# Performance work log

Measured on AMD Instinct MI355X. Metric: run time of the kernel, lower is better.

## Reference

```python
import jax, jax.numpy as jnp
import numpy as np

B, H, W, C = 32, 56, 56, 192
WS, SHIFT, HEADS = 7, 3, 6
HID = 4 * C
N = WS * WS
NW = (H // WS) * (W // WS)
EPS = 1e-5


def _rel_index():
    ch, cw = np.meshgrid(np.arange(WS), np.arange(WS), indexing='ij')
    coords = np.stack([ch.ravel(), cw.ravel()])  # [2, N]
    rel = coords[:, :, None] - coords[:, None, :]  # [2, N, N]
    rel = rel.transpose(1, 2, 0)
    rel[:, :, 0] += WS - 1
    rel[:, :, 1] += WS - 1
    rel[:, :, 0] *= 2 * WS - 1
    return rel.sum(-1).astype(np.int32)  # [N, N]


def _attn_mask():
    img = np.zeros((H, W), np.float32)
    sl = (slice(0, -WS), slice(-WS, -SHIFT), slice(-SHIFT, None))
    cnt = 0
    for hs in sl:
        for ws_ in sl:
            img[hs, ws_] = cnt
            cnt += 1
    mw = img.reshape(H // WS, WS, W // WS, WS).transpose(0, 2, 1, 3).reshape(-1, N)
    m = mw[:, None, :] - mw[:, :, None]
    return np.where(m != 0, -100.0, 0.0).astype(np.float32)  # [NW, N, N]


def setup_inputs() -> dict:
    key = jax.random.key(0)
    ks = jax.random.split(key, 16)
    r = lambda k, s, sc: (jax.random.normal(k, s, jnp.float32) * sc)
    return {
        'x': r(ks[0], (B, H * W, C), 1.0),
        'norm1_w': jnp.ones((C,), jnp.float32),
        'norm1_b': jnp.zeros((C,), jnp.float32),
        'qkv_w': r(ks[1], (C, 3 * C), 0.02),
        'qkv_b': jnp.zeros((3 * C,), jnp.float32),
        'bias_table': r(ks[2], ((2 * WS - 1) ** 2, HEADS), 0.02),
        'proj_w': r(ks[3], (C, C), 0.02),
        'proj_b': jnp.zeros((C,), jnp.float32),
        'norm2_w': jnp.ones((C,), jnp.float32),
        'norm2_b': jnp.zeros((C,), jnp.float32),
        'fc1_w': r(ks[4], (C, HID), 0.02),
        'fc1_b': jnp.zeros((HID,), jnp.float32),
        'fc2_w': r(ks[5], (HID, C), 0.02),
        'fc2_b': jnp.zeros((C,), jnp.float32),
        'attn_mask': jnp.asarray(_attn_mask()),
        'rel_index': jnp.asarray(_rel_index()),
    }


def _ln(x, w, b):
    mu = jnp.mean(x, -1, keepdims=True)
    var = jnp.mean(jnp.square(x - mu), -1, keepdims=True)
    return (x - mu) * jax.lax.rsqrt(var + EPS) * w + b


def reference(x, norm1_w, norm1_b, qkv_w, qkv_b, bias_table, proj_w, proj_b,
              norm2_w, norm2_b, fc1_w, fc1_b, fc2_w, fc2_b, attn_mask, rel_index):
    shortcut = x
    h = _ln(x, norm1_w, norm1_b).reshape(B, H, W, C)
    # cyclic shift
    h = jnp.roll(h, shift=(-SHIFT, -SHIFT), axis=(1, 2))
    # window partition -> (B*NW, N, C)
    h = h.reshape(B, H // WS, WS, W // WS, WS, C).transpose(0, 1, 3, 2, 4, 5)
    h = h.reshape(B * NW, N, C)
    # attention
    qkv = (h @ qkv_w + qkv_b).reshape(B * NW, N, 3, HEADS, C // HEADS)
    qkv = qkv.transpose(2, 0, 3, 1, 4)  # [3, B_, heads, N, d]
    q, k, v = qkv[0], qkv[1], qkv[2]
    scale = (C // HEADS) ** -0.5
    attn = jnp.einsum('bhnd,bhmd->bhnm', q * scale, k)
    bias = bias_table[rel_index].transpose(2, 0, 1)  # [heads, N, N]
    attn = attn + bias[None]
    attn = attn.reshape(B, NW, HEADS, N, N) + attn_mask[None, :, None]
    attn = jax.nn.softmax(attn.reshape(B * NW, HEADS, N, N), axis=-1)
    o = jnp.einsum('bhnm,bhmd->bhnd', attn, v)
    o = o.transpose(0, 2, 1, 3).reshape(B * NW, N, C)
    o = o @ proj_w + proj_b
    # window reverse
    o = o.reshape(B, H // WS, W // WS, WS, WS, C).transpose(0, 1, 3, 2, 4, 5)
    o = o.reshape(B, H, W, C)
    o = jnp.roll(o, shift=(SHIFT, SHIFT), axis=(1, 2)).reshape(B, H * W, C)
    x = shortcut + o
    # MLP (exact GELU, like torch nn.GELU)
    m = _ln(x, norm2_w, norm2_b)
    m = jax.nn.gelu(m @ fc1_w + fc1_b, approximate=False) @ fc2_w + fc2_b
    return x + m
```

## Files before the change

kernel.cpp:

```cpp
#include <hip/hip_runtime.h>
#include <math.h>

#define B_    32
#define HH    56
#define WW_   56
#define C_    192
#define WS_   7
#define SHIFT_ 3
#define HEADS_ 6
#define DH    32
#define N_    49
#define NWIN  2048
#define ROWS  100352
#define HID_  768
#define QKVN  576

typedef __bf16 bfr;
typedef __bf16 bf8 __attribute__((ext_vector_type(8)));
typedef __bf16 bf4 __attribute__((ext_vector_type(4)));
typedef float  f32x4 __attribute__((ext_vector_type(4)));

#define MFMA16(a,b,c) __builtin_amdgcn_mfma_f32_16x16x32_bf16(a,b,c,0,0,0)

#define OQW   0
#define OPW   110592
#define OW1   147456
#define OW2   294912
#define OBM   442368
#define WTOT  442368
#define BMTOT 1572864

__global__ __launch_bounds__(256) void k_prep(
    const float* __restrict__ qkvw, const float* __restrict__ projw,
    const float* __restrict__ w1,   const float* __restrict__ w2,
    bfr* __restrict__ wsp)
{
  int idx = blockIdx.x*256 + threadIdx.x;
  if (idx >= WTOT) return;
  if (idx < OPW)      { int i=idx;      int n=i/192, k=i%192; wsp[idx] = (bfr)qkvw[k*QKVN + n]; }
  else if (idx < OW1) { int i=idx-OPW;  int n=i/192, k=i%192; wsp[idx] = (bfr)projw[k*C_ + n]; }
  else if (idx < OW2) { int i=idx-OW1;  int n=i/192, k=i%192; wsp[idx] = (bfr)w1[k*HID_ + n]; }
  else                { int i=idx-OW2;  int n=i/768, k=i%768; wsp[idx] = (bfr)w2[k*C_ + n]; }
}

__global__ __launch_bounds__(256) void k_prep2(
    const float* __restrict__ btab, const int* __restrict__ rel,
    const float* __restrict__ mask, bfr* __restrict__ bm)
{
  int idx = blockIdx.x*256 + threadIdx.x;
  if (idx >= BMTOT) return;
  int row = idx & 63, col = (idx>>6) & 63, wi = (idx>>12) & 63, head = idx>>18;
  float v = -1e30f;
  if (row < N_ && col < N_) {
    int e = row*N_ + col;
    v = btab[rel[e]*HEADS_ + head] + mask[(size_t)wi*N_*N_ + e];
  }
  bm[idx] = (bfr)v;
}

#define SM_HS 0
#define SM_QS 25600
#define SM_KS 34816
#define SM_VT 44032
#define SM_P  53248
#define SM_OV 62464
#define SM_SR 71680
#define SM1_TOT 71936
#define HSP 200

__global__ __launch_bounds__(256, 2) void k_attn(
    const float* __restrict__ x,
    const float* __restrict__ n1w, const float* __restrict__ n1b,
    const bfr*   __restrict__ wsp,
    const float* __restrict__ qkvb,
    const float* __restrict__ projb,
    float* __restrict__ out)
{
  __shared__ char smem[SM1_TOT];
  bfr*   hs    = (bfr*)(smem + SM_HS);
  bfr*   qs    = (bfr*)(smem + SM_QS);
  bfr*   ks    = (bfr*)(smem + SM_KS);
  bfr*   vT    = (bfr*)(smem + SM_VT);
  bfr*   P     = (bfr*)(smem + SM_P);
  bfr*   ov2   = (bfr*)(smem + SM_OV);
  int*   srows = (int*)(smem + SM_SR);
  float* pj    = (float*)smem;

  const f32x4 ZERO4 = {0.f, 0.f, 0.f, 0.f};

  int win  = blockIdx.x;
  int tid  = threadIdx.x;
  int lane = tid & 63, wave = tid >> 6;
  int ln15 = lane & 15, quad = lane >> 4;
  int wi   = win & 63;

  if (tid < N_) {
    int bb = win >> 6;
    int wh = wi >> 3, ww = wi & 7;
    int th = tid / WS_, tw = tid % WS_;
    int sh = wh*WS_ + th + SHIFT_; if (sh >= HH) sh -= HH;
    int sw = ww*WS_ + tw + SHIFT_; if (sw >= WW_) sw -= WW_;
    srows[tid] = bb*HH*WW_ + sh*WW_ + sw;
  }
  {
    int* hz = (int*)(hs + 49*HSP);
    for (int i = tid; i < 15*HSP/2; i += 256) hz[i] = 0;
  }
  __syncthreads();
  for (int r = wave; r < N_; r += 4) {
    const float* xr = x + (size_t)srows[r]*C_;
    float v0 = xr[lane], v1 = xr[lane+64], v2 = xr[lane+128];
    float s = v0+v1+v2, q = v0*v0+v1*v1+v2*v2;
    #pragma unroll
    for (int m = 32; m; m >>= 1) { s += __shfl_xor(s, m); q += __shfl_xor(q, m); }
    float mu = s*(1.f/C_), var = q*(1.f/C_) - mu*mu;
    float rs = rsqrtf(var + 1e-5f);
    hs[r*HSP + lane]     = (bfr)((v0-mu)*rs*n1w[lane]     + n1b[lane]);
    hs[r*HSP + lane+64]  = (bfr)((v1-mu)*rs*n1w[lane+64]  + n1b[lane+64]);
    hs[r*HSP + lane+128] = (bfr)((v2-mu)*rs*n1w[lane+128] + n1b[lane+128]);
  }
  __syncthreads();

  const bfr* qkvwT  = wsp + OQW;
  const bfr* projwT = wsp + OPW;
  const bfr* bmask  = wsp + OBM;

  f32x4 accp[3][4];
  #pragma unroll
  for (int j=0;j<3;j++)
    #pragma unroll
    for (int mt=0;mt<4;mt++) accp[j][mt] = ZERO4;

  for (int pair = 0; pair < 3; pair++) {
    {
      bf8 bw[3][6];
      float qb[3];
      #pragma unroll
      for (int j=0;j<3;j++) {
        const bfr* wb = qkvwT + (size_t)(j*192 + pair*64 + wave*16 + ln15)*192 + quad*8;
        #pragma unroll
        for (int kk=0;kk<6;kk++)
          bw[j][kk] = *(const bf8*)&wb[kk*32];
        qb[j] = qkvb[j*192 + pair*64 + wave*16 + ln15];
      }
      f32x4 acc[3][4];
      #pragma unroll
      for (int j=0;j<3;j++)
        #pragma unroll
        for (int mt=0;mt<4;mt++) acc[j][mt] = ZERO4;
      #pragma unroll
      for (int kk = 0; kk < 6; kk++) {
        bf8 afr[4];
        #pragma unroll
        for (int mt=0;mt<4;mt++)
          afr[mt] = *(const bf8*)&hs[(mt*16+ln15)*HSP + kk*32 + quad*8];
        #pragma unroll
        for (int j=0;j<3;j++)
          #pragma unroll
          for (int mt=0;mt<4;mt++) acc[j][mt] = MFMA16(afr[mt], bw[j][kk], acc[j][mt]);
      }
      int colp = wave*16 + ln15;
      int hl = colp >> 5, d = colp & 31;
      #pragma unroll
      for (int j=0;j<3;j++) {
        #pragma unroll
        for (int mt=0;mt<4;mt++)
          #pragma unroll
          for (int r=0;r<4;r++) {
            int row = mt*16 + quad*4 + r;
            float vv = acc[j][mt][r] + qb[j];
            if (j == 0)      qs[(hl*64+row)*36 + d] = (bfr)(vv*0.17677669529663689f);
            else if (j == 1) ks[(hl*64+row)*36 + d] = (bfr)vv;
            else             vT[(hl*32+d)*72 + row] = (bfr)vv;
          }
      }
    }
    __syncthreads();

    bf4 bm4[2][4];
    #pragma unroll
    for (int hl = 0; hl < 2; hl++) {
      const bfr* bmh = bmask + (((size_t)(pair*2+hl)*64 + wi) << 12);
      #pragma unroll
      for (int nt = 0; nt < 4; nt++)
        bm4[hl][nt] = *(const bf4*)&bmh[(nt*16 + ln15)*64 + wave*16 + quad*4];
    }

    float val[2][4][4];
    #pragma unroll
    for (int hl = 0; hl < 2; hl++) {
      bf8 aq = *(const bf8*)&qs[(hl*64 + wave*16 + ln15)*36 + quad*8];
      #pragma unroll
      for (int nt = 0; nt < 4; nt++) {
        f32x4 c;
        c[0] = (float)bm4[hl][nt][0]; c[1] = (float)bm4[hl][nt][1];
        c[2] = (float)bm4[hl][nt][2]; c[3] = (float)bm4[hl][nt][3];
        bf8 bk = *(const bf8*)&ks[(hl*64 + nt*16 + ln15)*36 + quad*8];
        c = MFMA16(aq, bk, c);
        #pragma unroll
        for (int r=0;r<4;r++) val[hl][nt][r] = c[r];
      }
    }

    bf8 pw[2][3];
    #pragma unroll
    for (int hl = 0; hl < 2; hl++)
      #pragma unroll
      for (int j = 0; j < 3; j++)
        pw[hl][j] = *(const bf8*)&projwT[(size_t)((wave*3+j)*16 + ln15)*192
                                         + (pair*2+hl)*32 + quad*8];

    #pragma unroll
    for (int hl = 0; hl < 2; hl++) {
      float mx[4], sum[4];
      #pragma unroll
      for (int r=0;r<4;r++) {
        mx[r] = fmaxf(fmaxf(val[hl][0][r], val[hl][1][r]), fmaxf(val[hl][2][r], val[hl][3][r]));
        #pragma unroll
        for (int m = 1; m < 16; m <<= 1) mx[r] = fmaxf(mx[r], __shfl_xor(mx[r], m));
      }
      #pragma unroll
      for (int nt=0;nt<4;nt++)
        #pragma unroll
        for (int r=0;r<4;r++) val[hl][nt][r] = __expf(val[hl][nt][r] - mx[r]);
      #pragma unroll
      for (int r=0;r<4;r++) {
        sum[r] = val[hl][0][r] + val[hl][1][r] + val[hl][2][r] + val[hl][3][r];
        #pragma unroll
        for (int m = 1; m < 16; m <<= 1) sum[r] += __shfl_xor(sum[r], m);
        sum[r] = 1.f / sum[r];
      }
      #pragma unroll
      for (int nt=0;nt<4;nt++)
        #pragma unroll
        for (int r=0;r<4;r++)
          P[(wave*16 + quad*4 + r)*72 + nt*16 + ln15] = (bfr)(val[hl][nt][r]*sum[r]);
      #pragma unroll
      for (int nt = 0; nt < 2; nt++) {
        f32x4 c = ZERO4;
        #pragma unroll
        for (int k0 = 0; k0 < 64; k0 += 32) {
          bf8 ap = *(const bf8*)&P[(wave*16 + ln15)*72 + k0 + quad*8];
          bf8 bv = *(const bf8*)&vT[(hl*32 + nt*16 + ln15)*72 + k0 + quad*8];
          c = MFMA16(ap, bv, c);
        }
        #pragma unroll
        for (int r=0;r<4;r++)
          ov2[(wave*16 + quad*4 + r)*72 + hl*36 + nt*16 + ln15] = (bfr)c[r];
      }
    }
    __syncthreads();

    #pragma unroll
    for (int hl = 0; hl < 2; hl++) {
      bf8 afr[4];
      #pragma unroll
      for (int mt=0;mt<4;mt++)
        afr[mt] = *(const bf8*)&ov2[(mt*16+ln15)*72 + hl*36 + quad*8];
      #pragma unroll
      for (int j=0;j<3;j++)
        #pragma unroll
        for (int mt=0;mt<4;mt++) accp[j][mt] = MFMA16(afr[mt], pw[hl][j], accp[j][mt]);
    }
  }

  __syncthreads();
  #pragma unroll
  for (int j=0;j<3;j++) {
    int col = (wave*3+j)*16 + ln15;
    float pb = projb[col];
    #pragma unroll
    for (int mt=0;mt<4;mt++)
      #pragma unroll
      for (int r=0;r<4;r++)
        pj[(mt*16 + quad*4 + r)*196 + col] = accp[j][mt][r] + pb;
  }
  __syncthreads();
  for (int idx = tid; idx < N_*C_; idx += 256) {
    int n = idx / C_, c = idx % C_;
    size_t gr = (size_t)srows[n]*C_ + c;
    out[gr] = x[gr] + pj[n*196 + c];
  }
}

#define SM2_TS  0
#define SM2_HID 25600
#define SM2_TOT 51200

__global__ __launch_bounds__(256, 2) void k_mlp(
    float* __restrict__ y,
    const float* __restrict__ n2w, const float* __restrict__ n2b,
    const bfr* __restrict__ wsp,
    const float* __restrict__ b1, const float* __restrict__ b2)
{
  __shared__ char smem[SM2_TOT];
  bfr*   ts   = (bfr*)(smem + SM2_TS);
  bfr*   hidc = (bfr*)(smem + SM2_HID);
  float* st   = (float*)smem;

  const f32x4 ZERO4 = {0.f, 0.f, 0.f, 0.f};

  int r0 = blockIdx.x * 64;
  int tid = threadIdx.x;
  int lane = tid & 63, wave = tid >> 6;
  int ln15 = lane & 15, quad = lane >> 4;

  #pragma unroll
  for (int i = 0; i < 16; i++) {
    int r = wave + i*4;
    const float* yr = y + (size_t)(r0 + r)*C_;
    float v0 = yr[lane], v1 = yr[lane+64], v2 = yr[lane+128];
    float s = v0+v1+v2, q = v0*v0+v1*v1+v2*v2;
    #pragma unroll
    for (int m = 32; m; m >>= 1) { s += __shfl_xor(s, m); q += __shfl_xor(q, m); }
    float mu = s*(1.f/C_), var = q*(1.f/C_) - mu*mu;
    float rs = rsqrtf(var + 1e-5f);
    ts[r*HSP + lane]     = (bfr)((v0-mu)*rs*n2w[lane]     + n2b[lane]);
    ts[r*HSP + lane+64]  = (bfr)((v1-mu)*rs*n2w[lane+64]  + n2b[lane+64]);
    ts[r*HSP + lane+128] = (bfr)((v2-mu)*rs*n2w[lane+128] + n2b[lane+128]);
  }
  __syncthreads();

  const bfr* w1T = wsp + OW1;
  const bfr* w2T = wsp + OW2;

  f32x4 accp[3][4];
  #pragma unroll
  for (int j=0;j<3;j++)
    #pragma unroll
    for (int mt=0;mt<4;mt++) accp[j][mt] = ZERO4;

  for (int c = 0; c < 4; c++) {
    bf8 wf1[3][6];
    float bb[3];
    #pragma unroll
    for (int j=0;j<3;j++) {
      const bfr* wb = w1T + (size_t)((c*12 + wave*3 + j)*16 + ln15)*192 + quad*8;
      #pragma unroll
      for (int kk=0;kk<6;kk++)
        wf1[j][kk] = *(const bf8*)&wb[kk*32];
      bb[j] = b1[c*192 + (wave*3+j)*16 + ln15];
    }
    f32x4 acc[3][4];
    #pragma unroll
    for (int j=0;j<3;j++)
      #pragma unroll
      for (int mt=0;mt<4;mt++) acc[j][mt] = ZERO4;
    #pragma unroll
    for (int kk = 0; kk < 6; kk++) {
      bf8 afr[4];
      #pragma unroll
      for (int mt=0;mt<4;mt++)
        afr[mt] = *(const bf8*)&ts[(mt*16+ln15)*HSP + kk*32 + quad*8];
      #pragma unroll
      for (int j=0;j<3;j++)
        #pragma unroll
        for (int mt=0;mt<4;mt++) acc[j][mt] = MFMA16(afr[mt], wf1[j][kk], acc[j][mt]);
    }
    bf8 wf2[3][6];
    #pragma unroll
    for (int j=0;j<3;j++) {
      const bfr* wb2 = w2T + (size_t)((wave*3+j)*16 + ln15)*768 + c*192 + quad*8;
      #pragma unroll
      for (int kk=0;kk<6;kk++)
        wf2[j][kk] = *(const bf8*)&wb2[kk*32];
      int colc = (wave*3 + j)*16 + ln15;
      #pragma unroll
      for (int mt=0;mt<4;mt++)
        #pragma unroll
        for (int r=0;r<4;r++) {
          int row = mt*16 + quad*4 + r;
          float g = acc[j][mt][r] + bb[j];
          float u = g*(1.5957691216f + 0.0713548170f*g*g);
          hidc[row*HSP + colc] = (bfr)(g / (1.f + __expf(-u)));
        }
    }
    __syncthreads();
    #pragma unroll
    for (int kk = 0; kk < 6; kk++) {
      bf8 afr[4];
      #pragma unroll
      for (int mt=0;mt<4;mt++)
        afr[mt] = *(const bf8*)&hidc[(mt*16+ln15)*HSP + kk*32 + quad*8];
      #pragma unroll
      for (int j=0;j<3;j++)
        #pragma unroll
        for (int mt=0;mt<4;mt++) accp[j][mt] = MFMA16(afr[mt], wf2[j][kk], accp[j][mt]);
    }
    __syncthreads();
  }

  #pragma unroll
  for (int j=0;j<3;j++) {
    int col = (wave*3+j)*16 + ln15;
    float bb2 = b2[col];
    #pragma unroll
    for (int mt=0;mt<4;mt++)
      #pragma unroll
      for (int r=0;r<4;r++) {
        int row = mt*16 + quad*4 + r;
        st[row*196 + col] = accp[j][mt][r] + bb2;
      }
  }
  __syncthreads();
  for (int idx = tid; idx < 64*C_; idx += 256) {
    int r = idx / C_, c = idx % C_;
    size_t gr = (size_t)(r0 + r)*C_ + c;
    y[gr] = y[gr] + st[r*196 + c];
  }
}

extern "C" void kernel_launch(void* const* d_in, const int* in_sizes, int n_in,
                              void* d_out, int out_size, void* d_ws, size_t ws_size,
                              hipStream_t stream) {
  const float* x     = (const float*)d_in[0];
  const float* n1w   = (const float*)d_in[1];
  const float* n1b   = (const float*)d_in[2];
  const float* qkvw  = (const float*)d_in[3];
  const float* qkvb  = (const float*)d_in[4];
  const float* btab  = (const float*)d_in[5];
  const float* projw = (const float*)d_in[6];
  const float* projb = (const float*)d_in[7];
  const float* n2w   = (const float*)d_in[8];
  const float* n2b   = (const float*)d_in[9];
  const float* w1    = (const float*)d_in[10];
  const float* b1    = (const float*)d_in[11];
  const float* w2    = (const float*)d_in[12];
  const float* b2    = (const float*)d_in[13];
  const float* mask  = (const float*)d_in[14];
  const int*   rel   = (const int*)d_in[15];
  float* out = (float*)d_out;
  bfr*   wsp = (bfr*)d_ws;

  k_prep<<<(WTOT+255)/256, 256, 0, stream>>>(qkvw, projw, w1, w2, wsp);
  k_prep2<<<(BMTOT+255)/256, 256, 0, stream>>>(btab, rel, mask, wsp + OBM);
  k_attn<<<NWIN, 256, 0, stream>>>(x, n1w, n1b, wsp, qkvb, projb, out);
  k_mlp<<<ROWS/64, 256, 0, stream>>>(out, n2w, n2b, wsp, b1, b2);
}
```

Measured before the change: 522.3 us.

## Shrink bias-mask table to four window classes and stream weights per k-step

Compresses the precomputed bias+mask table from 64 windows to 4 boundary classes per head, since only windows on the last row or column differ in the shift mask. Keeps x values in registers from the LayerNorm pass and reuses them for the residual writeback instead of re-reading global memory. Weight fragments in the QKV and both MLP GEMMs are now loaded per k-step rather than preloaded in bulk, which lowers register pressure at the cost of less load latency hiding. The MLP hidden buffer is double-buffered in LDS, removing one barrier per chunk but raising LDS use to 75KB, which may reduce occupancy.

```diff
diff --git a/kernel.cpp b/kernel.cpp
--- a/kernel.cpp
+++ b/kernel.cpp
@@ -28,7 +28,7 @@
 #define OW2   294912
 #define OBM   442368
 #define WTOT  442368
-#define BMTOT 1572864
+#define BMTOT 98304
 
 __global__ __launch_bounds__(256) void k_prep(
     const float* __restrict__ qkvw, const float* __restrict__ projw,
@@ -49,7 +49,9 @@
 {
   int idx = blockIdx.x*256 + threadIdx.x;
   if (idx >= BMTOT) return;
-  int row = idx & 63, col = (idx>>6) & 63, wi = (idx>>12) & 63, head = idx>>18;
+  int row = idx & 63, col = (idx>>6) & 63, cls = (idx>>12) & 3, head = idx>>14;
+  int wh = (cls & 2) ? 7 : 0, ww = (cls & 1) ? 7 : 0;
+  int wi = wh*8 + ww;
   float v = -1e30f;
   if (row < N_ && col < N_) {
     int e = row*N_ + col;
@@ -93,6 +95,7 @@
   int lane = tid & 63, wave = tid >> 6;
   int ln15 = lane & 15, quad = lane >> 4;
   int wi   = win & 63;
+  int cls  = (((wi>>3)==7) ? 2 : 0) + (((wi&7)==7) ? 1 : 0);
 
   if (tid < N_) {
     int bb = win >> 6;
@@ -107,17 +110,23 @@
     for (int i = tid; i < 15*HSP/2; i += 256) hz[i] = 0;
   }
   __syncthreads();
-  for (int r = wave; r < N_; r += 4) {
-    const float* xr = x + (size_t)srows[r]*C_;
-    float v0 = xr[lane], v1 = xr[lane+64], v2 = xr[lane+128];
-    float s = v0+v1+v2, q = v0*v0+v1*v1+v2*v2;
-    #pragma unroll
-    for (int m = 32; m; m >>= 1) { s += __shfl_xor(s, m); q += __shfl_xor(q, m); }
-    float mu = s*(1.f/C_), var = q*(1.f/C_) - mu*mu;
-    float rs = rsqrtf(var + 1e-5f);
-    hs[r*HSP + lane]     = (bfr)((v0-mu)*rs*n1w[lane]     + n1b[lane]);
-    hs[r*HSP + lane+64]  = (bfr)((v1-mu)*rs*n1w[lane+64]  + n1b[lane+64]);
-    hs[r*HSP + lane+128] = (bfr)((v2-mu)*rs*n1w[lane+128] + n1b[lane+128]);
+  float xv0[13], xv1[13], xv2[13];
+  #pragma unroll
+  for (int i = 0; i < 13; i++) {
+    int r = wave + i*4;
+    if (r < N_) {
+      const float* xr = x + (size_t)srows[r]*C_;
+      float v0 = xr[lane], v1 = xr[lane+64], v2 = xr[lane+128];
+      xv0[i] = v0; xv1[i] = v1; xv2[i] = v2;
+      float s = v0+v1+v2, q = v0*v0+v1*v1+v2*v2;
+      #pragma unroll
+      for (int m = 32; m; m >>= 1) { s += __shfl_xor(s, m); q += __shfl_xor(q, m); }
+      float mu = s*(1.f/C_), var = q*(1.f/C_) - mu*mu;
+      float rs = rsqrtf(var + 1e-5f);
+      hs[r*HSP + lane]     = (bfr)((v0-mu)*rs*n1w[lane]     + n1b[lane]);
+      hs[r*HSP + lane+64]  = (bfr)((v1-mu)*rs*n1w[lane+64]  + n1b[lane+64]);
+      hs[r*HSP + lane+128] = (bfr)((v2-mu)*rs*n1w[lane+128] + n1b[lane+128]);
+    }
   }
   __syncthreads();
 
@@ -133,16 +142,9 @@
 
   for (int pair = 0; pair < 3; pair++) {
     {
-      bf8 bw[3][6];
       float qb[3];
       #pragma unroll
-      for (int j=0;j<3;j++) {
-        const bfr* wb = qkvwT + (size_t)(j*192 + pair*64 + wave*16 + ln15)*192 + quad*8;
-        #pragma unroll
-        for (int kk=0;kk<6;kk++)
-          bw[j][kk] = *(const bf8*)&wb[kk*32];
-        qb[j] = qkvb[j*192 + pair*64 + wave*16 + ln15];
-      }
+      for (int j=0;j<3;j++) qb[j] = qkvb[j*192 + pair*64 + wave*16 + ln15];
       f32x4 acc[3][4];
       #pragma unroll
       for (int j=0;j<3;j++)
@@ -155,9 +157,12 @@
         for (int mt=0;mt<4;mt++)
           afr[mt] = *(const bf8*)&hs[(mt*16+ln15)*HSP + kk*32 + quad*8];
         #pragma unroll
-        for (int j=0;j<3;j++)
+        for (int j=0;j<3;j++) {
+          bf8 bw = *(const bf8*)&qkvwT[(size_t)(j*192 + pair*64 + wave*16 + ln15)*192
+                                       + kk*32 + quad*8];
           #pragma unroll
-          for (int mt=0;mt<4;mt++) acc[j][mt] = MFMA16(afr[mt], bw[j][kk], acc[j][mt]);
+          for (int mt=0;mt<4;mt++) acc[j][mt] = MFMA16(afr[mt], bw, acc[j][mt]);
+        }
       }
       int colp = wave*16 + ln15;
       int hl = colp >> 5, d = colp & 31;
@@ -180,7 +185,7 @@
     bf4 bm4[2][4];
     #pragma unroll
     for (int hl = 0; hl < 2; hl++) {
-      const bfr* bmh = bmask + (((size_t)(pair*2+hl)*64 + wi) << 12);
+      const bfr* bmh = bmask + (((size_t)(pair*2+hl)*4 + cls) << 12);
       #pragma unroll
       for (int nt = 0; nt < 4; nt++)
         bm4[hl][nt] = *(const bf4*)&bmh[(nt*16 + ln15)*64 + wave*16 + quad*4];
@@ -276,16 +281,21 @@
         pj[(mt*16 + quad*4 + r)*196 + col] = accp[j][mt][r] + pb;
   }
   __syncthreads();
-  for (int idx = tid; idx < N_*C_; idx += 256) {
-    int n = idx / C_, c = idx % C_;
-    size_t gr = (size_t)srows[n]*C_ + c;
-    out[gr] = x[gr] + pj[n*196 + c];
+  #pragma unroll
+  for (int i = 0; i < 13; i++) {
+    int r = wave + i*4;
+    if (r < N_) {
+      float* orow = out + (size_t)srows[r]*C_;
+      orow[lane]     = xv0[i] + pj[r*196 + lane];
+      orow[lane+64]  = xv1[i] + pj[r*196 + lane+64];
+      orow[lane+128] = xv2[i] + pj[r*196 + lane+128];
+    }
   }
 }
 
 #define SM2_TS  0
-#define SM2_HID 25600
-#define SM2_TOT 51200
+#define SM2_H0  25600
+#define SM2_TOT 76800
 
 __global__ __launch_bounds__(256, 2) void k_mlp(
     float* __restrict__ y,
@@ -294,9 +304,8 @@
     const float* __restrict__ b1, const float* __restrict__ b2)
 {
   __shared__ char smem[SM2_TOT];
-  bfr*   ts   = (bfr*)(smem + SM2_TS);
-  bfr*   hidc = (bfr*)(smem + SM2_HID);
-  float* st   = (float*)smem;
+  bfr*   ts  = (bfr*)(smem + SM2_TS);
+  float* st  = (float*)smem;
 
   const f32x4 ZERO4 = {0.f, 0.f, 0.f, 0.f};
 
@@ -305,9 +314,7 @@
   int lane = tid & 63, wave = tid >> 6;
   int ln15 = lane & 15, quad = lane >> 4;
 
-  #pragma unroll
-  for (int i = 0; i < 16; i++) {
-    int r = wave + i*4;
+  for (int r = wave; r < 64; r += 4) {
     const float* yr = y + (size_t)(r0 + r)*C_;
     float v0 = yr[lane], v1 = yr[lane+64], v2 = yr[lane+128];
     float s = v0+v1+v2, q = v0*v0+v1*v1+v2*v2;
@@ -331,63 +338,59 @@
     for (int mt=0;mt<4;mt++) accp[j][mt] = ZERO4;
 
   for (int c = 0; c < 4; c++) {
-    bf8 wf1[3][6];
-    float bb[3];
-    #pragma unroll
-    for (int j=0;j<3;j++) {
-      const bfr* wb = w1T + (size_t)((c*12 + wave*3 + j)*16 + ln15)*192 + quad*8;
-      #pragma unroll
-      for (int kk=0;kk<6;kk++)
-        wf1[j][kk] = *(const bf8*)&wb[kk*32];
-      bb[j] = b1[c*192 + (wave*3+j)*16 + ln15];
-    }
-    f32x4 acc[3][4];
-    #pragma unroll
-    for (int j=0;j<3;j++)
-      #pragma unroll
-      for (int mt=0;mt<4;mt++) acc[j][mt] = ZERO4;
+    bfr* hidc = (bfr*)(smem + SM2_H0 + (c & 1)*25600);
+    {
+      f32x4 acc[3][4];
+      #pragma unroll
+      for (int j=0;j<3;j++)
+        #pragma unroll
+        for (int mt=0;mt<4;mt++) acc[j][mt] = ZERO4;
+      float bb[3];
+      #pragma unroll
+      for (int j=0;j<3;j++) bb[j] = b1[c*192 + (wave*3+j)*16 + ln15];
+      #pragma unroll
+      for (int kk = 0; kk < 6; kk++) {
+        bf8 afr[4];
+        #pragma unroll
+        for (int mt=0;mt<4;mt++)
+          afr[mt] = *(const bf8*)&ts[(mt*16+ln15)*HSP + kk*32 + quad*8];
+        #pragma unroll
+        for (int j=0;j<3;j++) {
+          bf8 bw = *(const bf8*)&w1T[(size_t)((c*12 + wave*3 + j)*16 + ln15)*192
+                                     + kk*32 + quad*8];
+          #pragma unroll
+          for (int mt=0;mt<4;mt++) acc[j][mt] = MFMA16(afr[mt], bw, acc[j][mt]);
+        }
+      }
+      #pragma unroll
+      for (int j=0;j<3;j++) {
+        int colc = (wave*3 + j)*16 + ln15;
+        #pragma unroll
+        for (int mt=0;mt<4;mt++)
+          #pragma unroll
+          for (int r=0;r<4;r++) {
+            int row = mt*16 + quad*4 + r;
+            float g = acc[j][mt][r] + bb[j];
+            float u = g*(1.5957691216f + 0.0713548170f*g*g);
+            hidc[row*HSP + colc] = (bfr)(g / (1.f + __expf(-u)));
+          }
+      }
+    }
+    __syncthreads();
     #pragma unroll
     for (int kk = 0; kk < 6; kk++) {
       bf8 afr[4];
       #pragma unroll
       for (int mt=0;mt<4;mt++)
-        afr[mt] = *(const bf8*)&ts[(mt*16+ln15)*HSP + kk*32 + quad*8];
-      #pragma unroll
-      for (int j=0;j<3;j++)
-        #pragma unroll
-        for (int mt=0;mt<4;mt++) acc[j][mt] = MFMA16(afr[mt], wf1[j][kk], acc[j][mt]);
-    }
-    bf8 wf2[3][6];
-    #pragma unroll
-    for (int j=0;j<3;j++) {
-      const bfr* wb2 = w2T + (size_t)((wave*3+j)*16 + ln15)*768 + c*192 + quad*8;
-      #pragma unroll
-      for (int kk=0;kk<6;kk++)
-        wf2[j][kk] = *(const bf8*)&wb2[kk*32];
-      int colc = (wave*3 + j)*16 + ln15;
-      #pragma unroll
-      for (int mt=0;mt<4;mt++)
-        #pragma unroll
-        for (int r=0;r<4;r++) {
-          int row = mt*16 + quad*4 + r;
-          float g = acc[j][mt][r] + bb[j];
-          float u = g*(1.5957691216f + 0.0713548170f*g*g);
-          hidc[row*HSP + colc] = (bfr)(g / (1.f + __expf(-u)));
-        }
-    }
-    __syncthreads();
-    #pragma unroll
-    for (int kk = 0; kk < 6; kk++) {
-      bf8 afr[4];
-      #pragma unroll
-      for (int mt=0;mt<4;mt++)
         afr[mt] = *(const bf8*)&hidc[(mt*16+ln15)*HSP + kk*32 + quad*8];
       #pragma unroll
-      for (int j=0;j<3;j++)
-        #pragma unroll
-        for (int mt=0;mt<4;mt++) accp[j][mt] = MFMA16(afr[mt], wf2[j][kk], accp[j][mt]);
-    }
-    __syncthreads();
+      for (int j=0;j<3;j++) {
+        bf8 bw = *(const bf8*)&w2T[(size_t)((wave*3+j)*16 + ln15)*768
+                                   + c*192 + kk*32 + quad*8];
+        #pragma unroll
+        for (int mt=0;mt<4;mt++) accp[j][mt] = MFMA16(afr[mt], bw, accp[j][mt]);
+      }
+    }
   }
 
   #pragma unroll
```

After: 535.9 us. 1.03x slower.
